# Kernel tuning notes

Hardware: AMD Instinct MI355X
Metric: run time of the kernel (lower is better)

Reference implementation:

```python
import jax, jax.numpy as jnp
import numpy as np

N, D, H = 65536, 512, 256  # batch, input_dim, hidden_dim
BN_EPS = 1e-5
EPS = 1e-15


def setup_inputs() -> dict:
    key = jax.random.key(0)
    ks = jax.random.split(key, 10)
    rn = lambda k, shape, sc: jax.random.normal(k, shape, dtype=jnp.float32) * sc
    return {
        "x1": rn(ks[0], (N, D), 1.0),
        "x2": rn(ks[1], (N, D), 1.0),
        "W1": rn(ks[2], (D, H), 0.04),
        "b1": jnp.zeros((H,), jnp.float32),
        "gamma": jnp.ones((H,), jnp.float32),
        "beta_bn": jnp.zeros((H,), jnp.float32),
        "W2": rn(ks[3], (H, H // 2), 0.06),
        "b2": jnp.zeros((H // 2,), jnp.float32),
        "W3": rn(ks[4], (H // 2 * 3, 64), 0.05),
        "b3": jnp.zeros((64,), jnp.float32),
        "W4": rn(ks[5], (64, 1), 0.12),
        "b4": jnp.zeros((1,), jnp.float32),
        "alpha": jnp.array([0.65], jnp.float32),
        "beta": jnp.array([0.25], jnp.float32),
    }


def _proj(x, W1, b1, gamma, beta_bn, W2, b2):
    h = x @ W1 + b1                       # [N, 256]
    mean = jnp.mean(h, axis=0)
    var = jnp.var(h, axis=0)              # biased, matches BN training normalization
    h = gamma * (h - mean) * jax.lax.rsqrt(var + BN_EPS) + beta_bn
    h = jax.nn.relu(h)
    return jax.nn.relu(h @ W2 + b2)       # [N, 128]


def reference(x1, x2, W1, b1, gamma, beta_bn, W2, b2, W3, b3, W4, b4, alpha, beta):
    h1 = _proj(x1, W1, b1, gamma, beta_bn, W2, b2)
    h2 = _proj(x2, W1, b1, gamma, beta_bn, W2, b2)
    # diag of normalized similarity matrix == row-wise cosine similarity
    dot = jnp.sum(h1 * h2, axis=1)
    inv1 = 1.0 / jnp.maximum(jnp.sqrt(jnp.sum(h1 * h1, axis=1)), EPS)
    inv2 = 1.0 / jnp.maximum(jnp.sqrt(jnp.sum(h2 * h2, axis=1)), EPS)
    s_math = jnp.clip(dot * inv1 * inv2, 0.0, 1.0)
    combined = jnp.concatenate([h1 * h2, jnp.abs(h1 - h2), h1 + h2], axis=1)  # [N, 384]
    s_learn = (jax.nn.relu(combined @ W3 + b3) @ W4 + b4).reshape(-1)          # [N]
    final = alpha * s_math + beta * jax.nn.sigmoid(s_learn)
    return jnp.clip(final, 0.0, 1.0)
```

## Files before the change

### kernel.cpp

```cpp
#include <hip/hip_runtime.h>
#include <hip/hip_bf16.h>
#include <math.h>

#define NROWS 65536
#define DIN   512
#define H1    256
#define H2    128
#define K3DIM 384
#define O3    64

typedef short  short8  __attribute__((ext_vector_type(8)));
typedef float  f32x4   __attribute__((ext_vector_type(4)));
typedef unsigned short u16x4 __attribute__((ext_vector_type(4)));

__device__ __forceinline__ unsigned short f2bf(float f) {
    union { float f; unsigned int i; } v; v.f = f;
    unsigned int r = (v.i + 0x7fffu + ((v.i >> 16) & 1u)) >> 16;
    return (unsigned short)r;
}
__device__ __forceinline__ float bf2f(unsigned short u) {
    union { unsigned int i; float f; } v; v.i = ((unsigned int)u) << 16;
    return v.f;
}

__global__ void transpose_cvt_kernel(const float* __restrict__ src,
                                     unsigned short* __restrict__ dst, int R, int C) {
    int idx = blockIdx.x * 256 + threadIdx.x;
    if (idx >= R * C) return;
    int c = idx / R, r = idx - c * R;
    dst[idx] = f2bf(src[r * C + c]);
}

#define LDA 40

__global__ __launch_bounds__(256, 2)
void gemm1_kernel(const float* __restrict__ x1, const float* __restrict__ x2,
                  const unsigned short* __restrict__ w1t, const float* __restrict__ b1,
                  unsigned short* __restrict__ h_out) {
    __shared__ __align__(16) unsigned short Al[128 * LDA];
    __shared__ __align__(16) unsigned short Bl[128 * LDA];
    const int t  = threadIdx.x;
    const int n0 = blockIdx.x * 128;
    const int m0 = blockIdx.y * 128;
    const float* xp = (m0 < NROWS) ? x1 : x2;
    const int r0 = m0 & (NROWS - 1);

    const int wave = t >> 6, lane = t & 63;
    const int wm = wave >> 1, wn = wave & 1;
    const int m = lane & 15, q = lane >> 4;

    f32x4 acc[4][4] = {};

    for (int k0 = 0; k0 < DIN; k0 += 32) {
        __syncthreads();
#pragma unroll
        for (int i = 0; i < 4; ++i) {
            int u = t + i * 256;
            int r = u >> 3, kq = u & 7;
            const float4 v = *reinterpret_cast<const float4*>(xp + (size_t)(r0 + r) * DIN + k0 + kq * 4);
            u16x4 b; b.x = f2bf(v.x); b.y = f2bf(v.y); b.z = f2bf(v.z); b.w = f2bf(v.w);
            *reinterpret_cast<u16x4*>(&Al[r * LDA + kq * 4]) = b;
        }
        {
            int n = t >> 1, kh = t & 1;
            const float4* src = reinterpret_cast<const float4*>(w1t + (size_t)(n0 + n) * DIN + k0 + kh * 16);
            float4 v0 = src[0], v1 = src[1];
            *reinterpret_cast<float4*>(&Bl[n * LDA + kh * 16])     = v0;
            *reinterpret_cast<float4*>(&Bl[n * LDA + kh * 16 + 8]) = v1;
        }
        __syncthreads();
        short8 af[4], bfr[4];
#pragma unroll
        for (int mi = 0; mi < 4; ++mi)
            af[mi] = *reinterpret_cast<const short8*>(&Al[(wm * 64 + mi * 16 + m) * LDA + q * 8]);
#pragma unroll
        for (int ni = 0; ni < 4; ++ni)
            bfr[ni] = *reinterpret_cast<const short8*>(&Bl[(wn * 64 + ni * 16 + m) * LDA + q * 8]);
#pragma unroll
        for (int mi = 0; mi < 4; ++mi)
#pragma unroll
            for (int ni = 0; ni < 4; ++ni)
                acc[mi][ni] = __builtin_amdgcn_mfma_f32_16x16x32_bf16(af[mi], bfr[ni], acc[mi][ni], 0, 0, 0);
    }
#pragma unroll
    for (int mi = 0; mi < 4; ++mi)
#pragma unroll
        for (int ni = 0; ni < 4; ++ni) {
            int col = n0 + wn * 64 + ni * 16 + m;
            float bias = b1[col];
#pragma unroll
            for (int r = 0; r < 4; ++r) {
                int row = m0 + wm * 64 + mi * 16 + q * 4 + r;
                h_out[(size_t)row * H1 + col] = f2bf(acc[mi][ni][r] + bias);
            }
        }
}

__global__ void stats_kernel(const unsigned short* __restrict__ h, float* __restrict__ stats) {
    int b = blockIdx.x;
    int inp = b >> 8, chunk = b & 255;
    int col = threadIdx.x;
    const unsigned short* p = h + ((size_t)(inp * NROWS + chunk * 256)) * H1 + col;
    float s = 0.f, ss = 0.f;
    for (int i = 0; i < 256; ++i) {
        float v = bf2f(p[(size_t)i * H1]);
        s += v; ss += v * v;
    }
    atomicAdd(&stats[(inp * 2 + 0) * H1 + col], s);
    atomicAdd(&stats[(inp * 2 + 1) * H1 + col], ss);
}

__global__ void bnparams_kernel(const float* __restrict__ stats, const float* __restrict__ gamma,
                                const float* __restrict__ beta_bn, float* __restrict__ ab) {
    int t = threadIdx.x;
    int inp = t >> 8, c = t & 255;
    float mean = stats[(inp * 2 + 0) * H1 + c] * (1.0f / NROWS);
    float ex2  = stats[(inp * 2 + 1) * H1 + c] * (1.0f / NROWS);
    float var  = ex2 - mean * mean;
    float a = gamma[c] * rsqrtf(var + 1e-5f);
    ab[(inp * 2 + 0) * H1 + c] = a;
    ab[(inp * 2 + 1) * H1 + c] = beta_bn[c] - a * mean;
}

#define LDB2 264

__global__ __launch_bounds__(256, 2)
void gemm2_kernel(const unsigned short* __restrict__ h, const unsigned short* __restrict__ w2t,
                  const float* __restrict__ b2, const float* __restrict__ ab,
                  unsigned short* __restrict__ z) {
    __shared__ __align__(16) unsigned short Al[128 * LDA];
    __shared__ __align__(16) unsigned short B2[128 * LDB2];
    __shared__ float sc[H1], sh[H1];
    const int t  = threadIdx.x;
    const int m0 = blockIdx.x * 128;
    const int inp = m0 >> 16;
    if (t < 256) { sc[t] = ab[(inp * 2 + 0) * H1 + t]; sh[t] = ab[(inp * 2 + 1) * H1 + t]; }
#pragma unroll
    for (int i = 0; i < 8; ++i) {
        int c = t + i * 256;
        int n = c >> 4, kc = c & 15;
        const float4* src = reinterpret_cast<const float4*>(w2t + n * H1 + kc * 16);
        float4 v0 = src[0], v1 = src[1];
        *reinterpret_cast<float4*>(&B2[n * LDB2 + kc * 16])     = v0;
        *reinterpret_cast<float4*>(&B2[n * LDB2 + kc * 16 + 8]) = v1;
    }
    const int wave = t >> 6, lane = t & 63;
    const int wm = wave >> 1, wn = wave & 1;
    const int m = lane & 15, q = lane >> 4;
    f32x4 acc[4][4] = {};
    for (int k0 = 0; k0 < H1; k0 += 32) {
        __syncthreads();
        {
            int r = t >> 1, kh = t & 1;
            const unsigned short* src = h + (size_t)(m0 + r) * H1 + k0 + kh * 16;
            unsigned short vs[16]  __attribute__((aligned(16)));
            unsigned short ob[16]  __attribute__((aligned(16)));
            *reinterpret_cast<float4*>(vs)     = *reinterpret_cast<const float4*>(src);
            *reinterpret_cast<float4*>(vs + 8) = *reinterpret_cast<const float4*>(src + 8);
#pragma unroll
            for (int j = 0; j < 16; ++j) {
                int k = k0 + kh * 16 + j;
                float v = sc[k] * bf2f(vs[j]) + sh[k];
                ob[j] = f2bf(fmaxf(v, 0.f));
            }
            *reinterpret_cast<float4*>(&Al[r * LDA + kh * 16])     = *reinterpret_cast<float4*>(ob);
            *reinterpret_cast<float4*>(&Al[r * LDA + kh * 16 + 8]) = *reinterpret_cast<float4*>(ob + 8);
        }
        __syncthreads();
        short8 af[4], bfr[4];
#pragma unroll
        for (int mi = 0; mi < 4; ++mi)
            af[mi] = *reinterpret_cast<const short8*>(&Al[(wm * 64 + mi * 16 + m) * LDA + q * 8]);
#pragma unroll
        for (int ni = 0; ni < 4; ++ni)
            bfr[ni] = *reinterpret_cast<const short8*>(&B2[(wn * 64 + ni * 16 + m) * LDB2 + k0 + q * 8]);
#pragma unroll
        for (int mi = 0; mi < 4; ++mi)
#pragma unroll
            for (int ni = 0; ni < 4; ++ni)
                acc[mi][ni] = __builtin_amdgcn_mfma_f32_16x16x32_bf16(af[mi], bfr[ni], acc[mi][ni], 0, 0, 0);
    }
#pragma unroll
    for (int mi = 0; mi < 4; ++mi)
#pragma unroll
        for (int ni = 0; ni < 4; ++ni) {
            int col = wn * 64 + ni * 16 + m;
            float bias = b2[col];
#pragma unroll
            for (int r = 0; r < 4; ++r) {
                int row = m0 + wm * 64 + mi * 16 + q * 4 + r;
                z[(size_t)row * H2 + col] = f2bf(fmaxf(acc[mi][ni][r] + bias, 0.f));
            }
        }
}

#define LDZ  136
#define LDW3 392

__global__ __launch_bounds__(512, 2)
void head_kernel(const unsigned short* __restrict__ z, const unsigned short* __restrict__ w3t,
                 const float* __restrict__ b3, const float* __restrict__ w4,
                 const float* __restrict__ b4, const float* __restrict__ alpha,
                 const float* __restrict__ beta, float* __restrict__ out) {
    __shared__ __align__(16) unsigned short Z1[128 * LDZ];
    __shared__ __align__(16) unsigned short Z2[128 * LDZ];
    __shared__ __align__(16) unsigned short W3l[64 * LDW3];
    __shared__ float b3s[64], w4s[64];
    __shared__ float smath[128], slearn[128];

    const int t  = threadIdx.x;
    const int r0 = blockIdx.x * 128;

    {
        int r = t >> 2, seg = t & 3;
        const float4* f1 = reinterpret_cast<const float4*>(z + (size_t)(r0 + r) * H2 + seg * 32);
        const float4* f2 = reinterpret_cast<const float4*>(z + (size_t)(NROWS + r0 + r) * H2 + seg * 32);
        float4* d1 = reinterpret_cast<float4*>(&Z1[r * LDZ + seg * 32]);
        float4* d2 = reinterpret_cast<float4*>(&Z2[r * LDZ + seg * 32]);
        d1[0] = f1[0]; d1[1] = f1[1]; d1[2] = f1[2]; d1[3] = f1[3];
        d2[0] = f2[0]; d2[1] = f2[1]; d2[2] = f2[2]; d2[3] = f2[3];
    }
#pragma unroll
    for (int i = 0; i < 3; ++i) {
        int c = t + i * 512;
        int n = c / 24, kc = c - n * 24;
        const float4* src = reinterpret_cast<const float4*>(w3t + n * K3DIM + kc * 16);
        float4 v0 = src[0], v1 = src[1];
        *reinterpret_cast<float4*>(&W3l[n * LDW3 + kc * 16])     = v0;
        *reinterpret_cast<float4*>(&W3l[n * LDW3 + kc * 16 + 8]) = v1;
    }
    if (t < 64) { b3s[t] = b3[t]; w4s[t] = w4[t]; }
    __syncthreads();

    {
        int r = t >> 2, part = t & 3;
        float d = 0.f, s1 = 0.f, s2 = 0.f;
#pragma unroll
        for (int j = 0; j < 32; ++j) {
            int k = part * 32 + j;
            float a = bf2f(Z1[r * LDZ + k]);
            float b = bf2f(Z2[r * LDZ + k]);
            d += a * b; s1 += a * a; s2 += b * b;
        }
        d  += __shfl_xor(d, 1);  d  += __shfl_xor(d, 2);
        s1 += __shfl_xor(s1, 1); s1 += __shfl_xor(s1, 2);
        s2 += __shfl_xor(s2, 1); s2 += __shfl_xor(s2, 2);
        if (part == 0) {
            float inv1 = 1.f / fmaxf(sqrtf(s1), 1e-15f);
            float inv2 = 1.f / fmaxf(sqrtf(s2), 1e-15f);
            float sm = d * inv1 * inv2;
            smath[r] = fminf(fmaxf(sm, 0.f), 1.f);
        }
    }

    const int wave = t >> 6, lane = t & 63;
    const int m = lane & 15, q = lane >> 4;
    const int wr = wave * 16;
    f32x4 acc[4] = {};
#pragma unroll
    for (int kb = 0; kb < 12; ++kb) {
        int seg = kb >> 2;
        int kl  = (kb & 3) * 32 + q * 8;
        short8 a1 = *reinterpret_cast<const short8*>(&Z1[(wr + m) * LDZ + kl]);
        short8 a2 = *reinterpret_cast<const short8*>(&Z2[(wr + m) * LDZ + kl]);
        short8 af;
#pragma unroll
        for (int j = 0; j < 8; ++j) {
            float v1 = bf2f((unsigned short)a1[j]);
            float v2 = bf2f((unsigned short)a2[j]);
            float v = (seg == 0) ? v1 * v2 : (seg == 1 ? fabsf(v1 - v2) : v1 + v2);
            af[j] = (short)f2bf(v);
        }
#pragma unroll
        for (int ni = 0; ni < 4; ++ni) {
            short8 bfr = *reinterpret_cast<const short8*>(&W3l[(ni * 16 + m) * LDW3 + kb * 32 + q * 8]);
            acc[ni] = __builtin_amdgcn_mfma_f32_16x16x32_bf16(af, bfr, acc[ni], 0, 0, 0);
        }
    }
    float partial[4] = {0.f, 0.f, 0.f, 0.f};
#pragma unroll
    for (int ni = 0; ni < 4; ++ni) {
        int col = ni * 16 + m;
        float bias = b3s[col], w4v = w4s[col];
#pragma unroll
        for (int rg = 0; rg < 4; ++rg) {
            float v = fmaxf(acc[ni][rg] + bias, 0.f);
            partial[rg] += v * w4v;
        }
    }
#pragma unroll
    for (int rg = 0; rg < 4; ++rg) {
        float p = partial[rg];
        p += __shfl_xor(p, 1); p += __shfl_xor(p, 2);
        p += __shfl_xor(p, 4); p += __shfl_xor(p, 8);
        if (m == 0) slearn[wr + q * 4 + rg] = p + b4[0];
    }
    __syncthreads();
    if (t < 128) {
        float sl = slearn[t];
        float sig = 1.f / (1.f + expf(-sl));
        float f = alpha[0] * smath[t] + beta[0] * sig;
        out[r0 + t] = fminf(fmaxf(f, 0.f), 1.f);
    }
}

extern "C" void kernel_launch(void* const* d_in, const int* in_sizes, int n_in,
                              void* d_out, int out_size, void* d_ws, size_t ws_size,
                              hipStream_t stream) {
    (void)in_sizes; (void)n_in; (void)out_size; (void)ws_size;
    const float* x1      = (const float*)d_in[0];
    const float* x2      = (const float*)d_in[1];
    const float* W1      = (const float*)d_in[2];
    const float* b1      = (const float*)d_in[3];
    const float* gamma   = (const float*)d_in[4];
    const float* beta_bn = (const float*)d_in[5];
    const float* W2      = (const float*)d_in[6];
    const float* b2      = (const float*)d_in[7];
    const float* W3      = (const float*)d_in[8];
    const float* b3      = (const float*)d_in[9];
    const float* W4      = (const float*)d_in[10];
    const float* b4      = (const float*)d_in[11];
    const float* alpha   = (const float*)d_in[12];
    const float* beta    = (const float*)d_in[13];
    float* out = (float*)d_out;

    char* ws = (char*)d_ws;
    unsigned short* h   = (unsigned short*)(ws);
    unsigned short* w1t = (unsigned short*)(ws + 67108864);
    unsigned short* w2t = (unsigned short*)(ws + 67371008);
    unsigned short* w3t = (unsigned short*)(ws + 67436544);
    float*          stats = (float*)(ws + 67485696);
    float*          ab    = (float*)(ws + 67489792);
    unsigned short* z   = (unsigned short*)(ws + 67493888);

    (void)hipMemsetAsync(stats, 0, 4096, stream);
    transpose_cvt_kernel<<<(DIN * H1 + 255) / 256, 256, 0, stream>>>(W1, w1t, DIN, H1);
    transpose_cvt_kernel<<<(H1 * H2 + 255) / 256, 256, 0, stream>>>(W2, w2t, H1, H2);
    transpose_cvt_kernel<<<(K3DIM * O3 + 255) / 256, 256, 0, stream>>>(W3, w3t, K3DIM, O3);
    gemm1_kernel<<<dim3(2, 1024), 256, 0, stream>>>(x1, x2, w1t, b1, h);
    stats_kernel<<<512, 256, 0, stream>>>(h, stats);
    bnparams_kernel<<<1, 512, 0, stream>>>(stats, gamma, beta_bn, ab);
    gemm2_kernel<<<1024, 256, 0, stream>>>(h, w2t, b2, ab, z);
    head_kernel<<<512, 512, 0, stream>>>(z, w3t, b3, W4, b4, alpha, beta, out);
}
```

Before: 397.5 us.

## Fuse BN stats into GEMM1, prefetch tiles, merge weight prep, register-stage head

Folds the batch-norm column sum and sum-of-squares into the GEMM1 epilogue using shuffles and atomics, which removes the separate stats pass over h. Both GEMMs now prefetch the next K tile into registers during the MFMA work, and launch bounds go from 2 to 3 blocks per CU. The three weight transpose launches become one prep kernel. GEMM2 streams W2 per K tile instead of loading it all into LDS, and the head kernel reads z straight into registers and computes cosine similarity inside the MFMA loop. The risks are more atomic contention and register pressure under the tighter occupancy target, and the statistics are now summed in fp32 before bf16 rounding, which changes numerics slightly.

Result: slower. 454.4 us (+14.3%).

```diff
diff --git a/kernel.cpp b/kernel.cpp
--- a/kernel.cpp
+++ b/kernel.cpp
@@ -23,52 +23,78 @@
     return v.f;
 }
 
-__global__ void transpose_cvt_kernel(const float* __restrict__ src,
-                                     unsigned short* __restrict__ dst, int R, int C) {
+__global__ void prep_kernel(const float* __restrict__ W1, const float* __restrict__ W2,
+                            const float* __restrict__ W3,
+                            unsigned short* __restrict__ w1t, unsigned short* __restrict__ w2t,
+                            unsigned short* __restrict__ w3t) {
     int idx = blockIdx.x * 256 + threadIdx.x;
-    if (idx >= R * C) return;
-    int c = idx / R, r = idx - c * R;
-    dst[idx] = f2bf(src[r * C + c]);
+    if (idx < DIN * H1) {
+        int c = idx >> 9, r = idx & 511;
+        w1t[idx] = f2bf(W1[r * H1 + c]);
+    } else if (idx < DIN * H1 + H1 * H2) {
+        int i2 = idx - DIN * H1;
+        int c = i2 >> 8, r = i2 & 255;
+        w2t[i2] = f2bf(W2[r * H2 + c]);
+    } else if (idx < DIN * H1 + H1 * H2 + K3DIM * O3) {
+        int i3 = idx - DIN * H1 - H1 * H2;
+        int c = i3 / K3DIM, r = i3 - c * K3DIM;
+        w3t[i3] = f2bf(W3[r * O3 + c]);
+    }
 }
 
 #define LDA 40
 
-__global__ __launch_bounds__(256, 2)
+__global__ __launch_bounds__(256, 3)
 void gemm1_kernel(const float* __restrict__ x1, const float* __restrict__ x2,
                   const unsigned short* __restrict__ w1t, const float* __restrict__ b1,
-                  unsigned short* __restrict__ h_out) {
+                  unsigned short* __restrict__ h_out, float* __restrict__ stats) {
     __shared__ __align__(16) unsigned short Al[128 * LDA];
     __shared__ __align__(16) unsigned short Bl[128 * LDA];
     const int t  = threadIdx.x;
     const int n0 = blockIdx.x * 128;
     const int m0 = blockIdx.y * 128;
     const float* xp = (m0 < NROWS) ? x1 : x2;
+    const int inp = (m0 < NROWS) ? 0 : 1;
     const int r0 = m0 & (NROWS - 1);
 
     const int wave = t >> 6, lane = t & 63;
     const int wm = wave >> 1, wn = wave & 1;
     const int m = lane & 15, q = lane >> 4;
 
+    const int ar = t >> 1, ah = t & 1;
+    const float* abase = xp + (size_t)(r0 + ar) * DIN + ah * 16;
+    const unsigned short* bbase = w1t + (size_t)(n0 + ar) * DIN + ah * 16;
+
     f32x4 acc[4][4] = {};
+    float4 pa[4];
+    float4 pb[2];
+
+#pragma unroll
+    for (int i = 0; i < 4; ++i) pa[i] = *reinterpret_cast<const float4*>(abase + i * 4);
+    pb[0] = *reinterpret_cast<const float4*>(bbase);
+    pb[1] = *reinterpret_cast<const float4*>(bbase + 8);
 
     for (int k0 = 0; k0 < DIN; k0 += 32) {
         __syncthreads();
-#pragma unroll
-        for (int i = 0; i < 4; ++i) {
-            int u = t + i * 256;
-            int r = u >> 3, kq = u & 7;
-            const float4 v = *reinterpret_cast<const float4*>(xp + (size_t)(r0 + r) * DIN + k0 + kq * 4);
-            u16x4 b; b.x = f2bf(v.x); b.y = f2bf(v.y); b.z = f2bf(v.z); b.w = f2bf(v.w);
-            *reinterpret_cast<u16x4*>(&Al[r * LDA + kq * 4]) = b;
-        }
         {
-            int n = t >> 1, kh = t & 1;
-            const float4* src = reinterpret_cast<const float4*>(w1t + (size_t)(n0 + n) * DIN + k0 + kh * 16);
-            float4 v0 = src[0], v1 = src[1];
-            *reinterpret_cast<float4*>(&Bl[n * LDA + kh * 16])     = v0;
-            *reinterpret_cast<float4*>(&Bl[n * LDA + kh * 16 + 8]) = v1;
+            unsigned short ob[16] __attribute__((aligned(16)));
+#pragma unroll
+            for (int i = 0; i < 4; ++i) {
+                ob[4 * i + 0] = f2bf(pa[i].x); ob[4 * i + 1] = f2bf(pa[i].y);
+                ob[4 * i + 2] = f2bf(pa[i].z); ob[4 * i + 3] = f2bf(pa[i].w);
+            }
+            *reinterpret_cast<float4*>(&Al[ar * LDA + ah * 16])     = *reinterpret_cast<float4*>(ob);
+            *reinterpret_cast<float4*>(&Al[ar * LDA + ah * 16 + 8]) = *reinterpret_cast<float4*>(ob + 8);
+            *reinterpret_cast<float4*>(&Bl[ar * LDA + ah * 16])     = pb[0];
+            *reinterpret_cast<float4*>(&Bl[ar * LDA + ah * 16 + 8]) = pb[1];
         }
         __syncthreads();
+        if (k0 + 32 < DIN) {
+#pragma unroll
+            for (int i = 0; i < 4; ++i) pa[i] = *reinterpret_cast<const float4*>(abase + k0 + 32 + i * 4);
+            pb[0] = *reinterpret_cast<const float4*>(bbase + k0 + 32);
+            pb[1] = *reinterpret_cast<const float4*>(bbase + k0 + 32 + 8);
+        }
         short8 af[4], bfr[4];
 #pragma unroll
         for (int mi = 0; mi < 4; ++mi)
@@ -82,32 +108,36 @@
             for (int ni = 0; ni < 4; ++ni)
                 acc[mi][ni] = __builtin_amdgcn_mfma_f32_16x16x32_bf16(af[mi], bfr[ni], acc[mi][ni], 0, 0, 0);
     }
-#pragma unroll
-    for (int mi = 0; mi < 4; ++mi)
+
+    float s[4] = {0.f, 0.f, 0.f, 0.f}, ss[4] = {0.f, 0.f, 0.f, 0.f};
+#pragma unroll
+    for (int ni = 0; ni < 4; ++ni) {
+        int col = n0 + wn * 64 + ni * 16 + m;
+        float bias = b1[col];
+#pragma unroll
+        for (int mi = 0; mi < 4; ++mi) {
+#pragma unroll
+            for (int r = 0; r < 4; ++r) {
+                int row = m0 + wm * 64 + mi * 16 + q * 4 + r;
+                float v = acc[mi][ni][r] + bias;
+                h_out[(size_t)row * H1 + col] = f2bf(v);
+                s[ni] += v; ss[ni] += v * v;
+            }
+        }
+    }
+#pragma unroll
+    for (int ni = 0; ni < 4; ++ni) {
+        s[ni]  += __shfl_xor(s[ni], 16);  s[ni]  += __shfl_xor(s[ni], 32);
+        ss[ni] += __shfl_xor(ss[ni], 16); ss[ni] += __shfl_xor(ss[ni], 32);
+    }
+    if (q == 0) {
 #pragma unroll
         for (int ni = 0; ni < 4; ++ni) {
             int col = n0 + wn * 64 + ni * 16 + m;
-            float bias = b1[col];
-#pragma unroll
-            for (int r = 0; r < 4; ++r) {
-                int row = m0 + wm * 64 + mi * 16 + q * 4 + r;
-                h_out[(size_t)row * H1 + col] = f2bf(acc[mi][ni][r] + bias);
-            }
-        }
-}
-
-__global__ void stats_kernel(const unsigned short* __restrict__ h, float* __restrict__ stats) {
-    int b = blockIdx.x;
-    int inp = b >> 8, chunk = b & 255;
-    int col = threadIdx.x;
-    const unsigned short* p = h + ((size_t)(inp * NROWS + chunk * 256)) * H1 + col;
-    float s = 0.f, ss = 0.f;
-    for (int i = 0; i < 256; ++i) {
-        float v = bf2f(p[(size_t)i * H1]);
-        s += v; ss += v * v;
-    }
-    atomicAdd(&stats[(inp * 2 + 0) * H1 + col], s);
-    atomicAdd(&stats[(inp * 2 + 1) * H1 + col], ss);
+            atomicAdd(&stats[inp * 2 * H1 + col], s[ni]);
+            atomicAdd(&stats[inp * 2 * H1 + H1 + col], ss[ni]);
+        }
+    }
 }
 
 __global__ void bnparams_kernel(const float* __restrict__ stats, const float* __restrict__ gamma,
@@ -122,58 +152,66 @@
     ab[(inp * 2 + 1) * H1 + c] = beta_bn[c] - a * mean;
 }
 
-#define LDB2 264
-
-__global__ __launch_bounds__(256, 2)
+__global__ __launch_bounds__(256, 3)
 void gemm2_kernel(const unsigned short* __restrict__ h, const unsigned short* __restrict__ w2t,
                   const float* __restrict__ b2, const float* __restrict__ ab,
                   unsigned short* __restrict__ z) {
     __shared__ __align__(16) unsigned short Al[128 * LDA];
-    __shared__ __align__(16) unsigned short B2[128 * LDB2];
+    __shared__ __align__(16) unsigned short Bl[128 * LDA];
     __shared__ float sc[H1], sh[H1];
     const int t  = threadIdx.x;
     const int m0 = blockIdx.x * 128;
     const int inp = m0 >> 16;
-    if (t < 256) { sc[t] = ab[(inp * 2 + 0) * H1 + t]; sh[t] = ab[(inp * 2 + 1) * H1 + t]; }
-#pragma unroll
-    for (int i = 0; i < 8; ++i) {
-        int c = t + i * 256;
-        int n = c >> 4, kc = c & 15;
-        const float4* src = reinterpret_cast<const float4*>(w2t + n * H1 + kc * 16);
-        float4 v0 = src[0], v1 = src[1];
-        *reinterpret_cast<float4*>(&B2[n * LDB2 + kc * 16])     = v0;
-        *reinterpret_cast<float4*>(&B2[n * LDB2 + kc * 16 + 8]) = v1;
-    }
+    sc[t & 255] = ab[inp * 2 * H1 + (t & 255)];
+    sh[t & 255] = ab[inp * 2 * H1 + H1 + (t & 255)];
+
     const int wave = t >> 6, lane = t & 63;
     const int wm = wave >> 1, wn = wave & 1;
     const int m = lane & 15, q = lane >> 4;
+
+    const int ar = t >> 1, ah = t & 1;
+    const unsigned short* abase = h + (size_t)(m0 + ar) * H1 + ah * 16;
+    const unsigned short* bbase = w2t + (size_t)ar * H1 + ah * 16;
+
     f32x4 acc[4][4] = {};
+    float4 pa[2], pb[2];
+    pa[0] = *reinterpret_cast<const float4*>(abase);
+    pa[1] = *reinterpret_cast<const float4*>(abase + 8);
+    pb[0] = *reinterpret_cast<const float4*>(bbase);
+    pb[1] = *reinterpret_cast<const float4*>(bbase + 8);
+
     for (int k0 = 0; k0 < H1; k0 += 32) {
         __syncthreads();
         {
-            int r = t >> 1, kh = t & 1;
-            const unsigned short* src = h + (size_t)(m0 + r) * H1 + k0 + kh * 16;
-            unsigned short vs[16]  __attribute__((aligned(16)));
-            unsigned short ob[16]  __attribute__((aligned(16)));
-            *reinterpret_cast<float4*>(vs)     = *reinterpret_cast<const float4*>(src);
-            *reinterpret_cast<float4*>(vs + 8) = *reinterpret_cast<const float4*>(src + 8);
+            unsigned short vs[16] __attribute__((aligned(16)));
+            unsigned short ob[16] __attribute__((aligned(16)));
+            *reinterpret_cast<float4*>(vs)     = pa[0];
+            *reinterpret_cast<float4*>(vs + 8) = pa[1];
 #pragma unroll
             for (int j = 0; j < 16; ++j) {
-                int k = k0 + kh * 16 + j;
+                int k = k0 + ah * 16 + j;
                 float v = sc[k] * bf2f(vs[j]) + sh[k];
                 ob[j] = f2bf(fmaxf(v, 0.f));
             }
-            *reinterpret_cast<float4*>(&Al[r * LDA + kh * 16])     = *reinterpret_cast<float4*>(ob);
-            *reinterpret_cast<float4*>(&Al[r * LDA + kh * 16 + 8]) = *reinterpret_cast<float4*>(ob + 8);
+            *reinterpret_cast<float4*>(&Al[ar * LDA + ah * 16])     = *reinterpret_cast<float4*>(ob);
+            *reinterpret_cast<float4*>(&Al[ar * LDA + ah * 16 + 8]) = *reinterpret_cast<float4*>(ob + 8);
+            *reinterpret_cast<float4*>(&Bl[ar * LDA + ah * 16])     = pb[0];
+            *reinterpret_cast<float4*>(&Bl[ar * LDA + ah * 16 + 8]) = pb[1];
         }
         __syncthreads();
+        if (k0 + 32 < H1) {
+            pa[0] = *reinterpret_cast<const float4*>(abase + k0 + 32);
+            pa[1] = *reinterpret_cast<const float4*>(abase + k0 + 32 + 8);
+            pb[0] = *reinterpret_cast<const float4*>(bbase + k0 + 32);
+            pb[1] = *reinterpret_cast<const float4*>(bbase + k0 + 32 + 8);
+        }
         short8 af[4], bfr[4];
 #pragma unroll
         for (int mi = 0; mi < 4; ++mi)
             af[mi] = *reinterpret_cast<const short8*>(&Al[(wm * 64 + mi * 16 + m) * LDA + q * 8]);
 #pragma unroll
         for (int ni = 0; ni < 4; ++ni)
-            bfr[ni] = *reinterpret_cast<const short8*>(&B2[(wn * 64 + ni * 16 + m) * LDB2 + k0 + q * 8]);
+            bfr[ni] = *reinterpret_cast<const short8*>(&Bl[(wn * 64 + ni * 16 + m) * LDA + q * 8]);
 #pragma unroll
         for (int mi = 0; mi < 4; ++mi)
 #pragma unroll
@@ -194,16 +232,13 @@
         }
 }
 
-#define LDZ  136
 #define LDW3 392
 
-__global__ __launch_bounds__(512, 2)
+__global__ __launch_bounds__(512)
 void head_kernel(const unsigned short* __restrict__ z, const unsigned short* __restrict__ w3t,
                  const float* __restrict__ b3, const float* __restrict__ w4,
                  const float* __restrict__ b4, const float* __restrict__ alpha,
                  const float* __restrict__ beta, float* __restrict__ out) {
-    __shared__ __align__(16) unsigned short Z1[128 * LDZ];
-    __shared__ __align__(16) unsigned short Z2[128 * LDZ];
     __shared__ __align__(16) unsigned short W3l[64 * LDW3];
     __shared__ float b3s[64], w4s[64];
     __shared__ float smath[128], slearn[128];
@@ -211,15 +246,6 @@
     const int t  = threadIdx.x;
     const int r0 = blockIdx.x * 128;
 
-    {
-        int r = t >> 2, seg = t & 3;
-        const float4* f1 = reinterpret_cast<const float4*>(z + (size_t)(r0 + r) * H2 + seg * 32);
-        const float4* f2 = reinterpret_cast<const float4*>(z + (size_t)(NROWS + r0 + r) * H2 + seg * 32);
-        float4* d1 = reinterpret_cast<float4*>(&Z1[r * LDZ + seg * 32]);
-        float4* d2 = reinterpret_cast<float4*>(&Z2[r * LDZ + seg * 32]);
-        d1[0] = f1[0]; d1[1] = f1[1]; d1[2] = f1[2]; d1[3] = f1[3];
-        d2[0] = f2[0]; d2[1] = f2[1]; d2[2] = f2[2]; d2[3] = f2[3];
-    }
 #pragma unroll
     for (int i = 0; i < 3; ++i) {
         int c = t + i * 512;
@@ -232,43 +258,32 @@
     if (t < 64) { b3s[t] = b3[t]; w4s[t] = w4[t]; }
     __syncthreads();
 
-    {
-        int r = t >> 2, part = t & 3;
-        float d = 0.f, s1 = 0.f, s2 = 0.f;
-#pragma unroll
-        for (int j = 0; j < 32; ++j) {
-            int k = part * 32 + j;
-            float a = bf2f(Z1[r * LDZ + k]);
-            float b = bf2f(Z2[r * LDZ + k]);
-            d += a * b; s1 += a * a; s2 += b * b;
-        }
-        d  += __shfl_xor(d, 1);  d  += __shfl_xor(d, 2);
-        s1 += __shfl_xor(s1, 1); s1 += __shfl_xor(s1, 2);
-        s2 += __shfl_xor(s2, 1); s2 += __shfl_xor(s2, 2);
-        if (part == 0) {
-            float inv1 = 1.f / fmaxf(sqrtf(s1), 1e-15f);
-            float inv2 = 1.f / fmaxf(sqrtf(s2), 1e-15f);
-            float sm = d * inv1 * inv2;
-            smath[r] = fminf(fmaxf(sm, 0.f), 1.f);
-        }
-    }
-
     const int wave = t >> 6, lane = t & 63;
     const int m = lane & 15, q = lane >> 4;
     const int wr = wave * 16;
+    const int row = r0 + wr + m;
+
+    short8 z1c[4], z2c[4];
+#pragma unroll
+    for (int c = 0; c < 4; ++c) {
+        z1c[c] = *reinterpret_cast<const short8*>(z + (size_t)row * H2 + c * 32 + q * 8);
+        z2c[c] = *reinterpret_cast<const short8*>(z + (size_t)(NROWS + row) * H2 + c * 32 + q * 8);
+    }
+
+    float d = 0.f, s1 = 0.f, s2 = 0.f;
     f32x4 acc[4] = {};
 #pragma unroll
     for (int kb = 0; kb < 12; ++kb) {
-        int seg = kb >> 2;
-        int kl  = (kb & 3) * 32 + q * 8;
-        short8 a1 = *reinterpret_cast<const short8*>(&Z1[(wr + m) * LDZ + kl]);
-        short8 a2 = *reinterpret_cast<const short8*>(&Z2[(wr + m) * LDZ + kl]);
+        int seg = kb >> 2, c = kb & 3;
         short8 af;
 #pragma unroll
         for (int j = 0; j < 8; ++j) {
-            float v1 = bf2f((unsigned short)a1[j]);
-            float v2 = bf2f((unsigned short)a2[j]);
-            float v = (seg == 0) ? v1 * v2 : (seg == 1 ? fabsf(v1 - v2) : v1 + v2);
+            float v1 = bf2f((unsigned short)z1c[c][j]);
+            float v2 = bf2f((unsigned short)z2c[c][j]);
+            float v;
+            if (seg == 0) { v = v1 * v2; d += v; s1 += v1 * v1; s2 += v2 * v2; }
+            else if (seg == 1) v = fabsf(v1 - v2);
+            else v = v1 + v2;
             af[j] = (short)f2bf(v);
         }
 #pragma unroll
@@ -277,6 +292,15 @@
             acc[ni] = __builtin_amdgcn_mfma_f32_16x16x32_bf16(af, bfr, acc[ni], 0, 0, 0);
         }
     }
+    d  += __shfl_xor(d, 16);  d  += __shfl_xor(d, 32);
+    s1 += __shfl_xor(s1, 16); s1 += __shfl_xor(s1, 32);
+    s2 += __shfl_xor(s2, 16); s2 += __shfl_xor(s2, 32);
+    if (q == 0) {
+        float inv1 = 1.f / fmaxf(sqrtf(s1), 1e-15f);
+        float inv2 = 1.f / fmaxf(sqrtf(s2), 1e-15f);
+        smath[wr + m] = fminf(fmaxf(d * inv1 * inv2, 0.f), 1.f);
+    }
+
     float partial[4] = {0.f, 0.f, 0.f, 0.f};
 #pragma unroll
     for (int ni = 0; ni < 4; ++ni) {
@@ -334,11 +358,8 @@
     unsigned short* z   = (unsigned short*)(ws + 67493888);
 
     (void)hipMemsetAsync(stats, 0, 4096, stream);
-    transpose_cvt_kernel<<<(DIN * H1 + 255) / 256, 256, 0, stream>>>(W1, w1t, DIN, H1);
-    transpose_cvt_kernel<<<(H1 * H2 + 255) / 256, 256, 0, stream>>>(W2, w2t, H1, H2);
-    transpose_cvt_kernel<<<(K3DIM * O3 + 255) / 256, 256, 0, stream>>>(W3, w3t, K3DIM, O3);
-    gemm1_kernel<<<dim3(2, 1024), 256, 0, stream>>>(x1, x2, w1t, b1, h);
-    stats_kernel<<<512, 256, 0, stream>>>(h, stats);
+    prep_kernel<<<(DIN * H1 + H1 * H2 + K3DIM * O3 + 255) / 256, 256, 0, stream>>>(W1, W2, W3, w1t, w2t, w3t);
+    gemm1_kernel<<<dim3(2, 1024), 256, 0, stream>>>(x1, x2, w1t, b1, h, stats);
     bnparams_kernel<<<1, 512, 0, stream>>>(stats, gamma, beta_bn, ab);
     gemm2_kernel<<<1024, 256, 0, stream>>>(h, w2t, b2, ab, z);
     head_kernel<<<512, 512, 0, stream>>>(z, w3t, b3, W4, b4, alpha, beta, out);
```
